# Kernel tuning notes

Measured on AMD Instinct MI355X. Metric: run time of the kernel, lower is better.

The kernel has to match this reference:

```python
import jax, jax.numpy as jnp
import numpy as np

NUM_HEADS = 8
HEAD_SPLITS = [2, 3, 3]   # heads per conv window group (windows 3,5,7)


def _dwconv(x, w, b):
    # depthwise conv2d, SAME padding; x [B,Cg,H,W], w [Cg,1,k,k]
    k = w.shape[-1]
    pad = k // 2
    out = jax.lax.conv_general_dilated(
        x, w, window_strides=(1, 1), padding=[(pad, pad), (pad, pad)],
        feature_group_count=x.shape[1])
    return out + b[None, :, None, None]


def setup_inputs() -> dict:
    key = jax.random.key(0)
    ks = jax.random.split(key, 8)
    B, Hs, Ws, C = 16, 56, 56, 512
    N = 1 + Hs * Ws
    Ch = C // NUM_HEADS
    inp = {
        "x": jax.random.normal(ks[0], (B, N, C), dtype=jnp.float32),
        "qkv_w": jax.random.normal(ks[1], (3 * C, C), dtype=jnp.float32) * 0.02,
        "qkv_b": jnp.zeros((3 * C,), dtype=jnp.float32),
        "proj_w": jax.random.normal(ks[2], (C, C), dtype=jnp.float32) * 0.02,
        "proj_b": jnp.zeros((C,), dtype=jnp.float32),
        "conv_w3": jax.random.normal(ks[3], (2 * Ch, 1, 3, 3), dtype=jnp.float32) * 0.1,
        "conv_b3": jnp.zeros((2 * Ch,), dtype=jnp.float32),
        "conv_w5": jax.random.normal(ks[4], (3 * Ch, 1, 5, 5), dtype=jnp.float32) * 0.1,
        "conv_b5": jnp.zeros((3 * Ch,), dtype=jnp.float32),
        "conv_w7": jax.random.normal(ks[5], (3 * Ch, 1, 7, 7), dtype=jnp.float32) * 0.1,
        "conv_b7": jnp.zeros((3 * Ch,), dtype=jnp.float32),
        "H": 56,
        "W": 56,
    }
    return inp


def reference(x, qkv_w, qkv_b, proj_w, proj_b,
              conv_w3, conv_b3, conv_w5, conv_b5, conv_w7, conv_b7, H, W):
    B, N, C = x.shape
    h = NUM_HEADS
    Ch = C // h
    scale = Ch ** -0.5

    # qkv projection -> [3, B, h, N, Ch]
    qkv = (x @ qkv_w.T + qkv_b).reshape(B, N, 3, h, Ch)
    qkv = jnp.transpose(qkv, (2, 0, 3, 1, 4))
    q, k, v = qkv[0], qkv[1], qkv[2]

    # linear-attention factorization: softmax over tokens, then small Ch x Ch matmuls
    k_sm = jax.nn.softmax(k, axis=2)                     # softmax over N
    kv = jnp.einsum('bhnk,bhnd->bhkd', k_sm, v)          # [B,h,Ch,Ch]
    factor_att = jnp.einsum('bhnk,bhkd->bhnd', q, kv)    # [B,h,N,Ch]

    # conv relative-position encoding (CoaT ConvRelPosEnc)
    q_img = q[:, :, 1:, :]                               # drop CLS token
    v_img = v[:, :, 1:, :]
    v_img = jnp.transpose(v_img, (0, 1, 3, 2)).reshape(B, h * Ch, H, W)
    splits = np.cumsum([s * Ch for s in HEAD_SPLITS])[:-1]
    p3, p5, p7 = jnp.split(v_img, splits, axis=1)
    conv_v = jnp.concatenate([
        _dwconv(p3, conv_w3, conv_b3),
        _dwconv(p5, conv_w5, conv_b5),
        _dwconv(p7, conv_w7, conv_b7)], axis=1)           # [B,h*Ch,H,W]
    conv_v = jnp.transpose(conv_v.reshape(B, h, Ch, H * W), (0, 1, 3, 2))
    ev = q_img * conv_v                                   # [B,h,HW,Ch]
    crpe = jnp.concatenate(
        [jnp.zeros((B, h, 1, Ch), dtype=x.dtype), ev], axis=2)

    out = scale * factor_att + crpe                       # [B,h,N,Ch]
    out = jnp.transpose(out, (0, 2, 1, 3)).reshape(B, N, C)
    return out @ proj_w.T + proj_b
```

## Files before the change

### kernel.cpp

```cpp
#include <hip/hip_runtime.h>
#include <stdint.h>

#define NHEADS 8
#define NTOK   3137
#define BATCH  16
#define CDIM   512
#define MT     (BATCH*NTOK)

typedef unsigned short u16;
typedef float f32x4  __attribute__((ext_vector_type(4)));
typedef short bf16x8 __attribute__((ext_vector_type(8)));

__device__ __forceinline__ float bf2f(u16 u){
  union { uint32_t i; float f; } x; x.i = ((uint32_t)u) << 16; return x.f;
}
__device__ __forceinline__ u16 f2bf(float f){
  union { float f; uint32_t i; } x; x.f = f;
  uint32_t r = x.i + 0x7fffu + ((x.i >> 16) & 1u);
  return (u16)(r >> 16);
}
__device__ __forceinline__ void async_ld16(void* lds, const void* g){
  __builtin_amdgcn_global_load_lds((const __attribute__((address_space(1))) void*)g,
                                   (__attribute__((address_space(3))) void*)lds, 16, 0, 0);
}

__global__ void cvt_kernel(const float* __restrict__ src, u16* __restrict__ dst, int n4){
  int i = blockIdx.x * blockDim.x + threadIdx.x;
  if (i < n4){
    float4 v = ((const float4*)src)[i];
    uint32_t lo = ((uint32_t)f2bf(v.y) << 16) | f2bf(v.x);
    uint32_t hi = ((uint32_t)f2bf(v.w) << 16) | f2bf(v.z);
    ((uint2*)dst)[i] = make_uint2(lo, hi);
  }
}

template<int BM,int BN,int WM,int WN,int MODE>
__global__ __launch_bounds__(WM*WN*64, 2) void gemm2(
    const u16* __restrict__ A, const u16* __restrict__ Bw, const float* __restrict__ bias,
    u16* __restrict__ q_s, u16* __restrict__ k_s, u16* __restrict__ v_s,
    float* __restrict__ outF, int M)
{
  constexpr int THREADS = WM*WN*64;
  constexpr int MF = BM/(WM*16);
  constexpr int NF = BN/(WN*16);
  constexpr int WROWS = BM/WM;
  constexpr int WCOLS = BN/WN;
  __shared__ __align__(16) u16 smem[2*(BM+BN)*64];

  const int t = threadIdx.x;
  const int w = t >> 6, l = t & 63;
  const int wr = w / WN, wc = w % WN;
  const int lr = l & 15, lg = l >> 4;

  const int nx = gridDim.x;
  const int nwg = nx * gridDim.y;
  const int orig = blockIdx.y * nx + blockIdx.x;
  const int q8 = nwg >> 3, r8 = nwg & 7;
  const int xcd = orig & 7;
  const int wgid = (xcd < r8 ? xcd*(q8+1) : r8*(q8+1) + (xcd-r8)*q8) + (orig >> 3);
  const int n0 = (wgid % nx) * BN;
  const int m0 = (wgid / nx) * BM;

  f32x4 acc[MF][NF];
#pragma unroll
  for (int i=0;i<MF;i++)
#pragma unroll
    for (int j=0;j<NF;j++) acc[i][j] = (f32x4){0.f,0.f,0.f,0.f};

  auto stage = [&](int bi, int k0){
    u16* da = smem + bi*(BM*64);
    u16* db = smem + 2*BM*64 + bi*(BN*64);
#pragma unroll
    for (int j=0;j<(BM*8)/THREADS;j++){
      int qc = t + THREADS*j;
      int R = qc >> 3, c = qc & 7;
      int cs = (c ^ (R & 7)) * 8;
      int ar = m0 + R; if (ar > M-1) ar = M-1;
      async_ld16(&da[qc*8], &A[(size_t)ar*512 + k0 + cs]);
    }
#pragma unroll
    for (int j=0;j<(BN*8)/THREADS;j++){
      int qc = t + THREADS*j;
      int R = qc >> 3, c = qc & 7;
      int cs = (c ^ (R & 7)) * 8;
      async_ld16(&db[qc*8], &Bw[(size_t)(n0+R)*512 + k0 + cs]);
    }
  };

  stage(0, 0);
  __syncthreads();
  int cur = 0;
  for (int kt = 0; kt < 8; ++kt){
    if (kt < 7) stage(cur ^ 1, (kt+1)*64);
    const u16* a_base = smem + cur*(BM*64);
    const u16* b_base = smem + 2*BM*64 + cur*(BN*64);
    __builtin_amdgcn_s_setprio(1);
#pragma unroll
    for (int ks=0; ks<2; ks++){
      bf16x8 af[MF], bfv[NF];
      int chunk = ks*4 + lg;
#pragma unroll
      for (int fi=0;fi<MF;fi++){
        int row = wr*WROWS + fi*16 + lr;
        af[fi] = *(const bf16x8*)&a_base[row*64 + ((chunk ^ (row & 7))*8)];
      }
#pragma unroll
      for (int fj=0;fj<NF;fj++){
        int col = wc*WCOLS + fj*16 + lr;
        bfv[fj] = *(const bf16x8*)&b_base[col*64 + ((chunk ^ (col & 7))*8)];
      }
#pragma unroll
      for (int fi=0;fi<MF;fi++)
#pragma unroll
        for (int fj=0;fj<NF;fj++)
          acc[fi][fj] = __builtin_amdgcn_mfma_f32_16x16x32_bf16(af[fi], bfv[fj], acc[fi][fj], 0, 0, 0);
    }
    __builtin_amdgcn_s_setprio(0);
    __syncthreads();
    cur ^= 1;
  }

  if (MODE == 0){
    u16* warea = smem + w * (WROWS*WCOLS);
    float bvv[NF];
#pragma unroll
    for (int fj=0;fj<NF;fj++) bvv[fj] = bias[n0 + wc*WCOLS + fj*16 + lr];
#pragma unroll
    for (int fi=0;fi<MF;fi++)
#pragma unroll
      for (int fj=0;fj<NF;fj++)
#pragma unroll
        for (int r=0;r<4;r++)
          warea[(fi*16 + lg*4 + r)*WCOLS + fj*16 + lr] = f2bf(acc[fi][fj][r] + bvv[fj]);
    __syncthreads();
    const int colo = n0 + wc*WCOLS;
    const int part = colo >> 9;
    const int hq   = (colo >> 6) & 7;
    u16* dst = (part == 0) ? q_s : ((part == 1) ? k_s : v_s);
    const int rsub = l >> 3;
    const int csub = (l & 7) * 8;
#pragma unroll
    for (int pass=0; pass<WROWS/8; ++pass){
      int rl = pass*8 + rsub;
      int m = m0 + wr*WROWS + rl;
      if (m < M){
        int bb = m / NTOK;
        int n  = m - bb*NTOK;
        uint4 vv = *(const uint4*)&warea[rl*WCOLS + csub];
        *(uint4*)&dst[((size_t)(bb*8 + hq)*NTOK + n)*64 + csub] = vv;
      }
    }
  } else {
    float* warea = (float*)smem + w * (WROWS*WCOLS);
    float bvv[NF];
#pragma unroll
    for (int fj=0;fj<NF;fj++) bvv[fj] = bias[n0 + wc*WCOLS + fj*16 + lr];
#pragma unroll
    for (int fi=0;fi<MF;fi++)
#pragma unroll
      for (int fj=0;fj<NF;fj++)
#pragma unroll
        for (int r=0;r<4;r++)
          warea[(fi*16 + lg*4 + r)*WCOLS + fj*16 + lr] = acc[fi][fj][r] + bvv[fj];
    __syncthreads();
    const int colo = n0 + wc*WCOLS;
    const int rsub = l >> 4;
    const int csub = (l & 15) * 4;
#pragma unroll
    for (int pass=0; pass<WROWS/4; ++pass){
      int rl = pass*4 + rsub;
      int m = m0 + wr*WROWS + rl;
      if (m < M){
        float4 vv = *(const float4*)&warea[rl*WCOLS + csub];
        *(float4*)&outF[(size_t)m*512 + colo + csub] = vv;
      }
    }
  }
}

__global__ __launch_bounds__(256) void kv_partial(
    const u16* __restrict__ k_s, const u16* __restrict__ v_s,
    float* __restrict__ kv_p, float* __restrict__ s_p)
{
  __shared__ float smem[18432];
  const int t  = threadIdx.x;
  const int bh = blockIdx.x;
  const int hf = blockIdx.y;
  const size_t base = (size_t)bh * NTOK * 64;
  const int srow = t >> 3;
  const int scol = (t & 7) * 8;
  const int ns = t >> 6;
  const int kg = (t >> 3) & 7;
  const int dg = t & 7;

  float accv[8][8];
#pragma unroll
  for (int a=0;a<8;a++)
#pragma unroll
    for (int c=0;c<8;c++) accv[a][c] = 0.f;
  float s_loc[8];
#pragma unroll
  for (int i=0;i<8;i++) s_loc[i] = 0.f;

  float* ek = smem;
  float* vv = smem + 2048;
  const int n_beg = hf * 1600;
  const int n_end = hf ? NTOK : 1600;

  for (int n0 = n_beg; n0 < n_end; n0 += 32){
    __syncthreads();
    int n = n0 + srow;
    float et[8], vf[8];
    if (n < n_end){
      uint4 kvec = *(const uint4*)&k_s[base + (size_t)n*64 + scol];
      uint4 vvec = *(const uint4*)&v_s[base + (size_t)n*64 + scol];
      const u16* kp = (const u16*)&kvec;
      const u16* vp = (const u16*)&vvec;
#pragma unroll
      for (int i=0;i<8;i++){
        et[i] = __expf(bf2f(kp[i]));
        s_loc[i] += et[i];
        vf[i] = bf2f(vp[i]);
      }
    } else {
#pragma unroll
      for (int i=0;i<8;i++){ et[i]=0.f; vf[i]=0.f; }
    }
    *(float4*)&ek[srow*64 + scol]     = make_float4(et[0],et[1],et[2],et[3]);
    *(float4*)&ek[srow*64 + scol + 4] = make_float4(et[4],et[5],et[6],et[7]);
    *(float4*)&vv[srow*64 + scol]     = make_float4(vf[0],vf[1],vf[2],vf[3]);
    *(float4*)&vv[srow*64 + scol + 4] = make_float4(vf[4],vf[5],vf[6],vf[7]);
    __syncthreads();
#pragma unroll
    for (int i=0;i<8;i++){
      int nl = ns + 4*i;
      float4 e0 = *(const float4*)&ek[nl*64 + kg*8];
      float4 e1 = *(const float4*)&ek[nl*64 + kg*8 + 4];
      float4 v0 = *(const float4*)&vv[nl*64 + dg*8];
      float4 v1 = *(const float4*)&vv[nl*64 + dg*8 + 4];
      float ea[8] = {e0.x,e0.y,e0.z,e0.w,e1.x,e1.y,e1.z,e1.w};
      float va[8] = {v0.x,v0.y,v0.z,v0.w,v1.x,v1.y,v1.z,v1.w};
#pragma unroll
      for (int a=0;a<8;a++)
#pragma unroll
        for (int c=0;c<8;c++) accv[a][c] += ea[a]*va[c];
    }
  }
  __syncthreads();
  float* part_kv = smem;
  float* part_s  = smem + 16384;
#pragma unroll
  for (int a=0;a<8;a++)
#pragma unroll
    for (int c=0;c<8;c++)
      part_kv[(size_t)ns*4096 + (kg*8+a)*64 + dg*8+c] = accv[a][c];
#pragma unroll
  for (int i=0;i<8;i++) part_s[srow*64 + scol + i] = s_loc[i];
  __syncthreads();
  const size_t obase = ((size_t)hf*128 + bh) * 4096;
  for (int i=0;i<16;i++){
    int e = t*16 + i;
    kv_p[obase + e] = part_kv[e] + part_kv[4096+e] + part_kv[8192+e] + part_kv[12288+e];
  }
  if (t < 64){
    float s = 0.f;
    for (int r=0;r<32;r++) s += part_s[r*64 + t];
    s_p[((size_t)hf*128 + bh)*64 + t] = s;
  }
}

__global__ void kv_reduce(const float* __restrict__ kv_p, const float* __restrict__ s_p,
                          u16* __restrict__ kvT){
  const int bh = blockIdx.x, t = threadIdx.x;
  for (int i=0;i<16;i++){
    int e = t*16 + i;
    int k = e >> 6, d = e & 63;
    float v = kv_p[(size_t)bh*4096 + e] + kv_p[(size_t)(128 + bh)*4096 + e];
    float S = s_p[bh*64 + k] + s_p[(128 + bh)*64 + k];
    kvT[(size_t)bh*4096 + d*64 + k] = f2bf(v / S);
  }
}

template<int R>
__global__ __launch_bounds__(256) void conv_ev(
    const u16* __restrict__ v_s, const u16* __restrict__ q_s,
    const float* __restrict__ wsrc, const float* __restrict__ bsrc,
    int h0, u16* __restrict__ out_pre)
{
  constexpr int KK = 2*R + 1;
  constexpr int TAPS = KK*KK;
  __shared__ __align__(16) u16 vt[KK*56*64];
  const int t = threadIdx.x;
  const int y = blockIdx.x;
  const int hh = blockIdx.y;
  const int b = blockIdx.z;
  const int h = h0 + hh;
  const size_t vbase = ((size_t)(b*8 + h)) * NTOK * 64;

  for (int ry=0; ry<KK; ry++){
    int yy = y - R + ry;
    for (int idx = t; idx < 448; idx += 256){
      uint4 val = make_uint4(0u,0u,0u,0u);
      if (yy >= 0 && yy < 56)
        val = *(const uint4*)&v_s[vbase + (size_t)(1 + yy*56)*64 + idx*8];
      *(uint4*)&vt[ry*3584 + idx*8] = val;
    }
  }
  __syncthreads();
  const int d = t & 63;
  const int xg = t >> 6;
  float wreg[TAPS];
#pragma unroll
  for (int i=0;i<TAPS;i++) wreg[i] = wsrc[(hh*64 + d)*TAPS + i];
  const float bias = bsrc[hh*64 + d];
  float acc[14];
#pragma unroll
  for (int i=0;i<14;i++) acc[i] = bias;
  const int x0 = xg * 14;
#pragma unroll
  for (int ry=0; ry<KK; ry++){
    float rw[14 + 2*R];
#pragma unroll
    for (int i=0; i<14+2*R; i++){
      int xx = x0 - R + i;
      rw[i] = (xx >= 0 && xx < 56) ? bf2f(vt[ry*3584 + xx*64 + d]) : 0.f;
    }
#pragma unroll
    for (int xi=0; xi<14; xi++)
#pragma unroll
      for (int rx=0; rx<KK; rx++)
        acc[xi] += rw[xi+rx] * wreg[ry*KK + rx];
  }
#pragma unroll
  for (int xi=0; xi<14; xi++){
    int x = x0 + xi;
    int n = 1 + y*56 + x;
    float qv = bf2f(q_s[vbase + (size_t)n*64 + d]);
    out_pre[((size_t)b*NTOK + n)*CDIM + h*64 + d] = f2bf(acc[xi] * qv);
  }
}

__global__ __launch_bounds__(256) void fa_add(
    const u16* __restrict__ q_s, const u16* __restrict__ kvT, u16* __restrict__ out_pre)
{
  __shared__ __align__(16) u16 sQ[64*64];
  __shared__ __align__(16) u16 sKV[64*64];
  const int t = threadIdx.x;
  const int nt = blockIdx.x;
  const int h = blockIdx.y;
  const int b = blockIdx.z;
  const int bh = b*8 + h;
  const size_t qbase = (size_t)bh * NTOK * 64;
  const int n0 = nt * 64;
#pragma unroll
  for (int j=0; j<2; j++){
    int qq = t + 256*j;
    int row = qq >> 3, c = qq & 7;
    int nrow = n0 + row; if (nrow > NTOK-1) nrow = NTOK-1;
    uint4 qv = *(const uint4*)&q_s[qbase + (size_t)nrow*64 + c*8];
    *(uint4*)&sQ[row*64 + ((c ^ (row & 7)) * 8)] = qv;
    uint4 kv = *(const uint4*)&kvT[(size_t)bh*4096 + row*64 + c*8];
    *(uint4*)&sKV[row*64 + ((c ^ (row & 7)) * 8)] = kv;
  }
  __syncthreads();
  const int w = t >> 6, l = t & 63, lr = l & 15, lg = l >> 4;
  f32x4 acc[4];
#pragma unroll
  for (int j=0;j<4;j++) acc[j] = (f32x4){0.f,0.f,0.f,0.f};
#pragma unroll
  for (int ks=0; ks<2; ks++){
    int chunk = ks*4 + lg;
    int arow = w*16 + lr;
    bf16x8 af = *(const bf16x8*)&sQ[arow*64 + ((chunk ^ (arow & 7))*8)];
#pragma unroll
    for (int fj=0; fj<4; fj++){
      int col = fj*16 + lr;
      bf16x8 bv = *(const bf16x8*)&sKV[col*64 + ((chunk ^ (col & 7))*8)];
      acc[fj] = __builtin_amdgcn_mfma_f32_16x16x32_bf16(af, bv, acc[fj], 0, 0, 0);
    }
  }
  const float scale = 0.125f;
#pragma unroll
  for (int fj=0; fj<4; fj++){
    int dcol = fj*16 + lr;
#pragma unroll
    for (int r=0; r<4; r++){
      int n = n0 + w*16 + lg*4 + r;
      if (n < NTOK){
        size_t addr = ((size_t)b*NTOK + n)*CDIM + h*64 + dcol;
        float prev = (n >= 1) ? bf2f(out_pre[addr]) : 0.f;
        out_pre[addr] = f2bf(scale*acc[fj][r] + prev);
      }
    }
  }
}

extern "C" void kernel_launch(void* const* d_in, const int* in_sizes, int n_in,
                              void* d_out, int out_size, void* d_ws, size_t ws_size,
                              hipStream_t stream)
{
  const float* x      = (const float*)d_in[0];
  const float* qkv_w  = (const float*)d_in[1];
  const float* qkv_b  = (const float*)d_in[2];
  const float* proj_w = (const float*)d_in[3];
  const float* proj_b = (const float*)d_in[4];
  const float* w3 = (const float*)d_in[5];
  const float* b3 = (const float*)d_in[6];
  const float* w5 = (const float*)d_in[7];
  const float* b5 = (const float*)d_in[8];
  const float* w7 = (const float*)d_in[9];
  const float* b7 = (const float*)d_in[10];
  float* out = (float*)d_out;

  char* ws = (char*)d_ws;
  size_t off = 0;
  auto alloc = [&](size_t bytes) -> void* {
    void* p = ws + off;
    off += (bytes + 255) & ~(size_t)255;
    return p;
  };
  u16*   x_bf     = (u16*)alloc((size_t)MT*512*2);
  u16*   qkvw_bf  = (u16*)alloc((size_t)1536*512*2);
  u16*   projw_bf = (u16*)alloc((size_t)512*512*2);
  u16*   q_s      = (u16*)alloc((size_t)128*NTOK*64*2);
  u16*   k_s      = (u16*)alloc((size_t)128*NTOK*64*2);
  u16*   v_s      = (u16*)alloc((size_t)128*NTOK*64*2);
  u16*   kvT      = (u16*)alloc((size_t)128*4096*2);
  float* kv_p     = (float*)alloc((size_t)2*128*4096*4);
  float* s_p      = (float*)alloc((size_t)2*128*64*4);
  u16*   out_pre  = x_bf;

  { int n4 = (MT*512)/4;   cvt_kernel<<<(n4+255)/256, 256, 0, stream>>>(x, x_bf, n4); }
  { int n4 = (1536*512)/4; cvt_kernel<<<(n4+255)/256, 256, 0, stream>>>(qkv_w, qkvw_bf, n4); }
  { int n4 = (512*512)/4;  cvt_kernel<<<(n4+255)/256, 256, 0, stream>>>(proj_w, projw_bf, n4); }

  gemm2<256,256,2,4,0><<<dim3(6, 197), 512, 0, stream>>>(
      x_bf, qkvw_bf, qkv_b, q_s, k_s, v_s, nullptr, MT);

  kv_partial<<<dim3(128, 2), 256, 0, stream>>>(k_s, v_s, kv_p, s_p);
  kv_reduce<<<128, 256, 0, stream>>>(kv_p, s_p, kvT);
  conv_ev<1><<<dim3(56, 2, 16), 256, 0, stream>>>(v_s, q_s, w3, b3, 0, out_pre);
  conv_ev<2><<<dim3(56, 3, 16), 256, 0, stream>>>(v_s, q_s, w5, b5, 2, out_pre);
  conv_ev<3><<<dim3(56, 3, 16), 256, 0, stream>>>(v_s, q_s, w7, b7, 5, out_pre);
  fa_add<<<dim3(50, 8, 16), 256, 0, stream>>>(q_s, kvT, out_pre);

  gemm2<128,128,2,2,1><<<dim3(4, 393), 256, 0, stream>>>(
      out_pre, projw_bf, proj_b, nullptr, nullptr, nullptr, out, MT);
}
```

Baseline: 392.9 us.

## Fuse factor-attention MFMA into conv kernels and split kv reduction four ways

The factor-attention product q·kvT now runs inside each depthwise-conv kernel, using a 56-token tile per image row. The fused result is written to out_pre once, which removes the separate fa_add pass and its read-modify-write of out_pre. The CLS token is handled by a small fa0_kernel. The kv_partial split also goes from 2 to 4 token ranges to raise parallelism, with kv_reduce summing four partials. The costs are more shared memory per conv block, an extra sync and LDS round-trip for the MFMA output, and a 64-row MFMA tile that only uses 56 rows.

```diff
diff --git a/kernel.cpp b/kernel.cpp
--- a/kernel.cpp
+++ b/kernel.cpp
@@ -23,6 +23,7 @@
   __builtin_amdgcn_global_load_lds((const __attribute__((address_space(1))) void*)g,
                                    (__attribute__((address_space(3))) void*)lds, 16, 0, 0);
 }
+#define MFMA16(d,a,b) d = __builtin_amdgcn_mfma_f32_16x16x32_bf16(a,b,d,0,0,0)
 
 __global__ void cvt_kernel(const float* __restrict__ src, u16* __restrict__ dst, int n4){
   int i = blockIdx.x * blockDim.x + threadIdx.x;
@@ -204,8 +205,8 @@
 
   float* ek = smem;
   float* vv = smem + 2048;
-  const int n_beg = hf * 1600;
-  const int n_end = hf ? NTOK : 1600;
+  const int n_beg = hf * 800;
+  const int n_end = (hf == 3) ? NTOK : (n_beg + 800);
 
   for (int n0 = n_beg; n0 < n_end; n0 += 32){
     __syncthreads();
@@ -275,47 +276,83 @@
   for (int i=0;i<16;i++){
     int e = t*16 + i;
     int k = e >> 6, d = e & 63;
-    float v = kv_p[(size_t)bh*4096 + e] + kv_p[(size_t)(128 + bh)*4096 + e];
-    float S = s_p[bh*64 + k] + s_p[(128 + bh)*64 + k];
+    float v = 0.f, S = 0.f;
+#pragma unroll
+    for (int hf=0; hf<4; hf++){
+      v += kv_p[(size_t)(hf*128 + bh)*4096 + e];
+      S += s_p[(hf*128 + bh)*64 + k];
+    }
     kvT[(size_t)bh*4096 + d*64 + k] = f2bf(v / S);
   }
 }
 
 template<int R>
-__global__ __launch_bounds__(256) void conv_ev(
+__global__ __launch_bounds__(256) void conv_fa(
     const u16* __restrict__ v_s, const u16* __restrict__ q_s,
+    const u16* __restrict__ kvT,
     const float* __restrict__ wsrc, const float* __restrict__ bsrc,
     int h0, u16* __restrict__ out_pre)
 {
   constexpr int KK = 2*R + 1;
   constexpr int TAPS = KK*KK;
-  __shared__ __align__(16) u16 vt[KK*56*64];
+  __shared__ __align__(16) u16 smem[8192 + KK*3584];
+  u16* vt = smem + 8192;
   const int t = threadIdx.x;
-  const int y = blockIdx.x;
+  const int y  = blockIdx.x;
   const int hh = blockIdx.y;
-  const int b = blockIdx.z;
-  const int h = h0 + hh;
-  const size_t vbase = ((size_t)(b*8 + h)) * NTOK * 64;
-
+  const int b  = blockIdx.z;
+  const int h  = h0 + hh;
+  const int bh = b*8 + h;
+  const size_t base = (size_t)bh * NTOK * 64;
+  const int n0 = 1 + y*56;
+
+#pragma unroll
+  for (int j=0;j<2;j++){
+    int qq = t + 256*j;
+    int row = qq >> 3, c = qq & 7;
+    int cs = (c ^ (row & 7)) * 8;
+    int n = n0 + row; if (n > NTOK-1) n = NTOK-1;
+    async_ld16(&smem[qq*8], &q_s[base + (size_t)n*64 + cs]);
+    async_ld16(&smem[4096 + qq*8], &kvT[(size_t)bh*4096 + row*64 + cs]);
+  }
   for (int ry=0; ry<KK; ry++){
     int yy = y - R + ry;
     for (int idx = t; idx < 448; idx += 256){
       uint4 val = make_uint4(0u,0u,0u,0u);
       if (yy >= 0 && yy < 56)
-        val = *(const uint4*)&v_s[vbase + (size_t)(1 + yy*56)*64 + idx*8];
+        val = *(const uint4*)&v_s[base + (size_t)(1 + yy*56)*64 + idx*8];
       *(uint4*)&vt[ry*3584 + idx*8] = val;
     }
   }
   __syncthreads();
-  const int d = t & 63;
-  const int xg = t >> 6;
+
+  const int w = t >> 6, l = t & 63;
+  const int lr = l & 15, lg = l >> 4;
+  f32x4 fac[4];
+#pragma unroll
+  for (int j=0;j<4;j++) fac[j] = (f32x4){0.f,0.f,0.f,0.f};
+#pragma unroll
+  for (int ks=0; ks<2; ks++){
+    int chunk = ks*4 + lg;
+    int arow = w*16 + lr;
+    bf16x8 af = *(const bf16x8*)&smem[arow*64 + ((chunk ^ (arow & 7))*8)];
+#pragma unroll
+    for (int fj=0; fj<4; fj++){
+      int col = fj*16 + lr;
+      bf16x8 bv = *(const bf16x8*)&smem[4096 + col*64 + ((chunk ^ (col & 7))*8)];
+      MFMA16(fac[fj], af, bv);
+    }
+  }
+
+  const int d = l;
+  const int xg = w;
   float wreg[TAPS];
 #pragma unroll
   for (int i=0;i<TAPS;i++) wreg[i] = wsrc[(hh*64 + d)*TAPS + i];
   const float bias = bsrc[hh*64 + d];
-  float acc[14];
-#pragma unroll
-  for (int i=0;i<14;i++) acc[i] = bias;
+  float creg[14];
+#pragma unroll
+  for (int i=0;i<14;i++) creg[i] = bias;
   const int x0 = xg * 14;
 #pragma unroll
   for (int ry=0; ry<KK; ry++){
@@ -329,70 +366,44 @@
     for (int xi=0; xi<14; xi++)
 #pragma unroll
       for (int rx=0; rx<KK; rx++)
-        acc[xi] += rw[xi+rx] * wreg[ry*KK + rx];
-  }
+        creg[xi] += rw[xi+rx] * wreg[ry*KK + rx];
+  }
+
+  float qv[14];
 #pragma unroll
   for (int xi=0; xi<14; xi++){
-    int x = x0 + xi;
-    int n = 1 + y*56 + x;
-    float qv = bf2f(q_s[vbase + (size_t)n*64 + d]);
-    out_pre[((size_t)b*NTOK + n)*CDIM + h*64 + d] = f2bf(acc[xi] * qv);
-  }
-}
-
-__global__ __launch_bounds__(256) void fa_add(
-    const u16* __restrict__ q_s, const u16* __restrict__ kvT, u16* __restrict__ out_pre)
-{
-  __shared__ __align__(16) u16 sQ[64*64];
-  __shared__ __align__(16) u16 sKV[64*64];
-  const int t = threadIdx.x;
-  const int nt = blockIdx.x;
-  const int h = blockIdx.y;
-  const int b = blockIdx.z;
+    int row = x0 + xi;
+    int chunk = d >> 3, e = d & 7;
+    qv[xi] = bf2f(smem[row*64 + ((chunk ^ (row & 7))*8) + e]);
+  }
+
+  __syncthreads();
+  float* fa = (float*)smem;
+#pragma unroll
+  for (int fj=0; fj<4; fj++)
+#pragma unroll
+    for (int r=0; r<4; r++)
+      fa[(w*16 + lg*4 + r)*64 + fj*16 + lr] = 0.125f * fac[fj][r];
+  __syncthreads();
+
+#pragma unroll
+  for (int xi=0; xi<14; xi++){
+    int nn = n0 + x0 + xi;
+    out_pre[((size_t)b*NTOK + nn)*CDIM + h*64 + d] =
+        f2bf(fa[(x0 + xi)*64 + d] + creg[xi]*qv[xi]);
+  }
+}
+
+__global__ void fa0_kernel(const u16* __restrict__ q_s, const u16* __restrict__ kvT,
+                           u16* __restrict__ out_pre){
+  const int b = blockIdx.x, t = threadIdx.x;
+  const int h = t >> 6, d = t & 63;
   const int bh = b*8 + h;
-  const size_t qbase = (size_t)bh * NTOK * 64;
-  const int n0 = nt * 64;
-#pragma unroll
-  for (int j=0; j<2; j++){
-    int qq = t + 256*j;
-    int row = qq >> 3, c = qq & 7;
-    int nrow = n0 + row; if (nrow > NTOK-1) nrow = NTOK-1;
-    uint4 qv = *(const uint4*)&q_s[qbase + (size_t)nrow*64 + c*8];
-    *(uint4*)&sQ[row*64 + ((c ^ (row & 7)) * 8)] = qv;
-    uint4 kv = *(const uint4*)&kvT[(size_t)bh*4096 + row*64 + c*8];
-    *(uint4*)&sKV[row*64 + ((c ^ (row & 7)) * 8)] = kv;
-  }
-  __syncthreads();
-  const int w = t >> 6, l = t & 63, lr = l & 15, lg = l >> 4;
-  f32x4 acc[4];
-#pragma unroll
-  for (int j=0;j<4;j++) acc[j] = (f32x4){0.f,0.f,0.f,0.f};
-#pragma unroll
-  for (int ks=0; ks<2; ks++){
-    int chunk = ks*4 + lg;
-    int arow = w*16 + lr;
-    bf16x8 af = *(const bf16x8*)&sQ[arow*64 + ((chunk ^ (arow & 7))*8)];
-#pragma unroll
-    for (int fj=0; fj<4; fj++){
-      int col = fj*16 + lr;
-      bf16x8 bv = *(const bf16x8*)&sKV[col*64 + ((chunk ^ (col & 7))*8)];
-      acc[fj] = __builtin_amdgcn_mfma_f32_16x16x32_bf16(af, bv, acc[fj], 0, 0, 0);
-    }
-  }
-  const float scale = 0.125f;
-#pragma unroll
-  for (int fj=0; fj<4; fj++){
-    int dcol = fj*16 + lr;
-#pragma unroll
-    for (int r=0; r<4; r++){
-      int n = n0 + w*16 + lg*4 + r;
-      if (n < NTOK){
-        size_t addr = ((size_t)b*NTOK + n)*CDIM + h*64 + dcol;
-        float prev = (n >= 1) ? bf2f(out_pre[addr]) : 0.f;
-        out_pre[addr] = f2bf(scale*acc[fj][r] + prev);
-      }
-    }
-  }
+  float s = 0.f;
+#pragma unroll
+  for (int k=0; k<64; k++)
+    s += bf2f(q_s[(size_t)bh*NTOK*64 + k]) * bf2f(kvT[(size_t)bh*4096 + d*64 + k]);
+  out_pre[(size_t)b*NTOK*CDIM + h*64 + d] = f2bf(0.125f * s);
 }
 
 extern "C" void kernel_launch(void* const* d_in, const int* in_sizes, int n_in,
@@ -426,8 +437,8 @@
   u16*   k_s      = (u16*)alloc((size_t)128*NTOK*64*2);
   u16*   v_s      = (u16*)alloc((size_t)128*NTOK*64*2);
   u16*   kvT      = (u16*)alloc((size_t)128*4096*2);
-  float* kv_p     = (float*)alloc((size_t)2*128*4096*4);
-  float* s_p      = (float*)alloc((size_t)2*128*64*4);
+  float* kv_p     = (float*)alloc((size_t)4*128*4096*4);
+  float* s_p      = (float*)alloc((size_t)4*128*64*4);
   u16*   out_pre  = x_bf;
 
   { int n4 = (MT*512)/4;   cvt_kernel<<<(n4+255)/256, 256, 0, stream>>>(x, x_bf, n4); }
@@ -437,12 +448,13 @@
   gemm2<256,256,2,4,0><<<dim3(6, 197), 512, 0, stream>>>(
       x_bf, qkvw_bf, qkv_b, q_s, k_s, v_s, nullptr, MT);
 
-  kv_partial<<<dim3(128, 2), 256, 0, stream>>>(k_s, v_s, kv_p, s_p);
+  kv_partial<<<dim3(128, 4), 256, 0, stream>>>(k_s, v_s, kv_p, s_p);
   kv_reduce<<<128, 256, 0, stream>>>(kv_p, s_p, kvT);
-  conv_ev<1><<<dim3(56, 2, 16), 256, 0, stream>>>(v_s, q_s, w3, b3, 0, out_pre);
-  conv_ev<2><<<dim3(56, 3, 16), 256, 0, stream>>>(v_s, q_s, w5, b5, 2, out_pre);
-  conv_ev<3><<<dim3(56, 3, 16), 256, 0, stream>>>(v_s, q_s, w7, b7, 5, out_pre);
-  fa_add<<<dim3(50, 8, 16), 256, 0, stream>>>(q_s, kvT, out_pre);
+  fa0_kernel<<<16, 512, 0, stream>>>(q_s, kvT, out_pre);
+
+  conv_fa<1><<<dim3(56, 2, 16), 256, 0, stream>>>(v_s, q_s, kvT, w3, b3, 0, out_pre);
+  conv_fa<2><<<dim3(56, 3, 16), 256, 0, stream>>>(v_s, q_s, kvT, w5, b5, 2, out_pre);
+  conv_fa<3><<<dim3(56, 3, 16), 256, 0, stream>>>(v_s, q_s, kvT, w7, b7, 5, out_pre);
 
   gemm2<128,128,2,2,1><<<dim3(4, 393), 256, 0, stream>>>(
       out_pre, projw_bf, proj_b, nullptr, nullptr, nullptr, out, MT);
```

Measured after the change: 378.2 us. 3.7% less time.
